# Kernel tuning notes

Measured on AMD Instinct MI355X. Metric: run time of the kernel, lower is better.

The kernel has to match this reference:

```python
import jax, jax.numpy as jnp
import numpy as np
from jax import lax

VOCAB = 32000
D = 64
B = 32
S = 512
DECAY_P = 0.1  # p in rho_t = (1-p)*rho_{t-1} + outer(x_t, x_t)


def setup_inputs() -> dict:
    key = jax.random.key(0)
    k1, k2 = jax.random.split(key)
    x = jax.random.randint(k1, (B, S), 0, VOCAB, dtype=jnp.int64)
    emb = jax.random.normal(k2, (VOCAB, D), dtype=jnp.float32)
    return {"x": x, "emb": emb}


def reference(x, emb):
    # Embedding lookup: [B, S, D]
    content = emb[x]
    # Per-token outer products (projectedRho): [B, S, D, D]
    proj = jnp.einsum('bsi,bsj->bsij', content, content)
    # Initial rho = identity, repeated over batch: [B, D, D]
    init_rho = jnp.broadcast_to(jnp.eye(D, dtype=emb.dtype), (B, D, D))
    decay = jnp.asarray(1.0 - DECAY_P, dtype=emb.dtype)

    def step(rho, p_t):
        rho = rho * decay + p_t  # [B, D, D]
        return rho, rho

    # scan over time axis; proj transposed to [S, B, D, D]
    _, states = lax.scan(step, init_rho, jnp.swapaxes(proj, 0, 1))
    # states: [S, B, D, D] -> return as [B, S, D, D] (stacked list of states)
    return jnp.swapaxes(states, 0, 1)
```

## Files before the change

kernel.cpp:

```cpp
#include <hip/hip_runtime.h>

#define VOCAB 32000
#define D     64
#define B     32
#define S     512
#define NCHUNK 8
#define CLEN   64

__device__ __constant__ const float DECAY = 0.9f;

__global__ void qmn_gather(const int* __restrict__ x,
                           const float4* __restrict__ emb4,
                           float4* __restrict__ content4) {
    int tid = blockIdx.x * blockDim.x + threadIdx.x;
    int bs  = tid >> 4;
    int d4  = tid & 15;
    int tok = x[bs];
    content4[tid] = emb4[tok * (D / 4) + d4];
}

__global__ void qmn_boundaries(const float* __restrict__ content,
                               float* __restrict__ bound) {
    int b     = blockIdx.x >> 4;
    int iBase = (blockIdx.x & 15) * 4;
    int j     = threadIdx.x & 63;
    int i     = iBase + (threadIdx.x >> 6);

    float rho = (i == j) ? 1.0f : 0.0f;
    const float* cb = content + (size_t)b * S * D;

    for (int t = 0; t < S; ++t) {
        float cj = cb[t * D + j];
        float ci = cb[t * D + i];
        rho = rho * DECAY + ci * cj;
        int tn = t + 1;
        if ((tn & (CLEN - 1)) == 0 && tn < S) {
            int c = tn >> 6;
            bound[(((size_t)b * NCHUNK + c) * D + i) * D + j] = rho;
        }
    }
}

__global__ void qmn_states(const float* __restrict__ content,
                           const float4* __restrict__ bound4,
                           float4* __restrict__ out4) {
    int blk   = blockIdx.x;
    int iBase = (blk & 3) * 16;
    int c     = (blk >> 2) & (NCHUNK - 1);
    int b     = blk >> 5;

    int jq = threadIdx.x & 15;
    int i  = iBase + (threadIdx.x >> 4);

    float4 rho;
    if (c == 0) {
        int j0 = jq * 4;
        rho.x = (i == j0 + 0) ? 1.0f : 0.0f;
        rho.y = (i == j0 + 1) ? 1.0f : 0.0f;
        rho.z = (i == j0 + 2) ? 1.0f : 0.0f;
        rho.w = (i == j0 + 3) ? 1.0f : 0.0f;
    } else {
        rho = bound4[(((size_t)b * NCHUNK + c) * D + i) * (D / 4) + jq];
    }

    const float*  cb  = content + ((size_t)b * S + (size_t)c * CLEN) * D;
    const float4* cb4 = (const float4*)cb;

    size_t outBase = ((size_t)b * S + (size_t)c * CLEN) * D;

    #pragma unroll 4
    for (int tt = 0; tt < CLEN; ++tt) {
        float  ci  = cb[tt * D + i];
        float4 cj4 = cb4[tt * (D / 4) + jq];
        rho.x = rho.x * DECAY + ci * cj4.x;
        rho.y = rho.y * DECAY + ci * cj4.y;
        rho.z = rho.z * DECAY + ci * cj4.z;
        rho.w = rho.w * DECAY + ci * cj4.w;
        out4[((outBase + (size_t)tt * D) + i) * (D / 4) + jq] = rho;
    }
}

extern "C" void kernel_launch(void* const* d_in, const int* in_sizes, int n_in,
                              void* d_out, int out_size, void* d_ws, size_t ws_size,
                              hipStream_t stream) {
    const int*   x   = (const int*)d_in[0];
    const float* emb = (const float*)d_in[1];
    float* out = (float*)d_out;

    float* content = (float*)d_ws;
    float* bound   = content + (size_t)B * S * D;

    {
        int total = B * S * (D / 4);
        qmn_gather<<<total / 256, 256, 0, stream>>>(x, (const float4*)emb,
                                                    (float4*)content);
    }
    qmn_boundaries<<<B * 16, 256, 0, stream>>>(content, bound);

    qmn_states<<<B * NCHUNK * 4, 256, 0, stream>>>(content, (const float4*)bound,
                                                   (float4*)out);
}
```

Before: 318.5 us.

## Fuse gather, boundary scan and state output into one kernel with redundant prefix recompute

Replaces the three-kernel pipeline (embedding gather, serial boundary scan, chunked state writes) with a single kernel. Each block recomputes its chunk's starting state by scanning all earlier tokens straight from the embedding table. This removes the long serial boundary kernel, the intermediate buffers and two launches, at the cost of redundant prefix work that grows with the chunk index. Output stores are now non-temporal to avoid polluting cache with the large write-only output.

```diff
diff --git a/kernel.cpp b/kernel.cpp
--- a/kernel.cpp
+++ b/kernel.cpp
@@ -7,76 +7,59 @@
 #define NCHUNK 8
 #define CLEN   64
 
-__device__ __constant__ const float DECAY = 0.9f;
+typedef float vf4 __attribute__((ext_vector_type(4)));
 
-__global__ void qmn_gather(const int* __restrict__ x,
-                           const float4* __restrict__ emb4,
-                           float4* __restrict__ content4) {
-    int tid = blockIdx.x * blockDim.x + threadIdx.x;
-    int bs  = tid >> 4;
-    int d4  = tid & 15;
-    int tok = x[bs];
-    content4[tid] = emb4[tok * (D / 4) + d4];
-}
+__global__ __launch_bounds__(256, 4) void qmn_fused(
+    const int*  __restrict__ x,
+    const float* __restrict__ emb,
+    vf4*        __restrict__ out4)
+{
+    const float DECAY = 0.9f;
 
-__global__ void qmn_boundaries(const float* __restrict__ content,
-                               float* __restrict__ bound) {
-    int b     = blockIdx.x >> 4;
-    int iBase = (blockIdx.x & 15) * 4;
-    int j     = threadIdx.x & 63;
-    int i     = iBase + (threadIdx.x >> 6);
-
-    float rho = (i == j) ? 1.0f : 0.0f;
-    const float* cb = content + (size_t)b * S * D;
-
-    for (int t = 0; t < S; ++t) {
-        float cj = cb[t * D + j];
-        float ci = cb[t * D + i];
-        rho = rho * DECAY + ci * cj;
-        int tn = t + 1;
-        if ((tn & (CLEN - 1)) == 0 && tn < S) {
-            int c = tn >> 6;
-            bound[(((size_t)b * NCHUNK + c) * D + i) * D + j] = rho;
-        }
-    }
-}
-
-__global__ void qmn_states(const float* __restrict__ content,
-                           const float4* __restrict__ bound4,
-                           float4* __restrict__ out4) {
     int blk   = blockIdx.x;
-    int iBase = (blk & 3) * 16;
-    int c     = (blk >> 2) & (NCHUNK - 1);
+    int c     = blk & (NCHUNK - 1);
+    int iBase = ((blk >> 3) & 3) * 16;
     int b     = blk >> 5;
 
     int jq = threadIdx.x & 15;
     int i  = iBase + (threadIdx.x >> 4);
 
-    float4 rho;
-    if (c == 0) {
-        int j0 = jq * 4;
-        rho.x = (i == j0 + 0) ? 1.0f : 0.0f;
-        rho.y = (i == j0 + 1) ? 1.0f : 0.0f;
-        rho.z = (i == j0 + 2) ? 1.0f : 0.0f;
-        rho.w = (i == j0 + 3) ? 1.0f : 0.0f;
-    } else {
-        rho = bound4[(((size_t)b * NCHUNK + c) * D + i) * (D / 4) + jq];
+    const int* xb = x + b * S;
+    const vf4* embv = (const vf4*)emb;
+
+    vf4 rho;
+    int j0 = jq * 4;
+    rho.x = (i == j0 + 0) ? 1.0f : 0.0f;
+    rho.y = (i == j0 + 1) ? 1.0f : 0.0f;
+    rho.z = (i == j0 + 2) ? 1.0f : 0.0f;
+    rho.w = (i == j0 + 3) ? 1.0f : 0.0f;
+
+    const int tStart = c * CLEN;
+
+    #pragma unroll 8
+    for (int t = 0; t < tStart; ++t) {
+        int tok = xb[t];
+        float ci = emb[tok * D + i];
+        vf4  cj  = embv[tok * (D / 4) + jq];
+        rho.x = rho.x * DECAY + ci * cj.x;
+        rho.y = rho.y * DECAY + ci * cj.y;
+        rho.z = rho.z * DECAY + ci * cj.z;
+        rho.w = rho.w * DECAY + ci * cj.w;
     }
 
-    const float*  cb  = content + ((size_t)b * S + (size_t)c * CLEN) * D;
-    const float4* cb4 = (const float4*)cb;
-
-    size_t outBase = ((size_t)b * S + (size_t)c * CLEN) * D;
+    vf4* outp = out4 + (((size_t)(b * S + tStart)) * D + i) * (D / 4) + jq;
 
     #pragma unroll 4
     for (int tt = 0; tt < CLEN; ++tt) {
-        float  ci  = cb[tt * D + i];
-        float4 cj4 = cb4[tt * (D / 4) + jq];
-        rho.x = rho.x * DECAY + ci * cj4.x;
-        rho.y = rho.y * DECAY + ci * cj4.y;
-        rho.z = rho.z * DECAY + ci * cj4.z;
-        rho.w = rho.w * DECAY + ci * cj4.w;
-        out4[((outBase + (size_t)tt * D) + i) * (D / 4) + jq] = rho;
+        int tok = xb[tStart + tt];
+        float ci = emb[tok * D + i];
+        vf4  cj  = embv[tok * (D / 4) + jq];
+        rho.x = rho.x * DECAY + ci * cj.x;
+        rho.y = rho.y * DECAY + ci * cj.y;
+        rho.z = rho.z * DECAY + ci * cj.z;
+        rho.w = rho.w * DECAY + ci * cj.w;
+        __builtin_nontemporal_store(rho, outp);
+        outp += D * (D / 4);
     }
 }
 
@@ -85,18 +68,7 @@
                               hipStream_t stream) {
     const int*   x   = (const int*)d_in[0];
     const float* emb = (const float*)d_in[1];
-    float* out = (float*)d_out;
+    vf4* out = (vf4*)d_out;
 
-    float* content = (float*)d_ws;
-    float* bound   = content + (size_t)B * S * D;
-
-    {
-        int total = B * S * (D / 4);
-        qmn_gather<<<total / 256, 256, 0, stream>>>(x, (const float4*)emb,
-                                                    (float4*)content);
-    }
-    qmn_boundaries<<<B * 16, 256, 0, stream>>>(content, bound);
-
-    qmn_states<<<B * NCHUNK * 4, 256, 0, stream>>>(content, (const float4*)bound,
-                                                   (float4*)out);
+    qmn_fused<<<B * NCHUNK * 4, 256, 0, stream>>>(x, emb, out);
 }
```

Result: slower. 365.4 us (+14.7%).
